# Kernel tuning notes

Hardware: AMD Instinct MI355X
Metric: run time of the kernel (lower is better)

## Reference

```python
import jax, jax.numpy as jnp
import numpy as np

LN_EPS = 1e-5

def _ln(x, g, b):
    m = jnp.mean(x, -1, keepdims=True)
    v = jnp.var(x, -1, keepdims=True)
    return (x - m) / jnp.sqrt(v + LN_EPS) * g + b

def _modgru(X, M, hx0, mask, Wcomb, bcomb, Wih, Whh, bih, bhh, Wc2, bc2):
    # X, M: [S,B,D]; hx0: [B,H]; mask: [S,B]
    # comb and the input-side gate GEMMs are hx-independent -> precompute over all steps
    comb = jnp.einsum('sbd,ed->sbe', jnp.concatenate([X, M], -1), Wcomb) + bcomb  # [S,B,D]
    gi = jnp.einsum('sbd,gd->sbg', comb, Wih) + bih  # [S,B,3H]

    def step(hx, inp):
        gi_t, m_t = inp
        gh = hx @ Whh.T + bhh
        ir, iz, inn = jnp.split(gi_t, 3, -1)
        hr, hz, hn = jnp.split(gh, 3, -1)
        r = jax.nn.sigmoid(ir + hr)
        z = jax.nn.sigmoid(iz + hz)
        n = jnp.tanh(inn + r * hn)
        hnew = (1.0 - z) * n + z * hx  # torch GRUCell update
        m = m_t[:, None]
        hx = hnew * m + hx * (1.0 - m)  # mask blending
        return hx, hx

    hx_last, hs = jax.lax.scan(step, hx0, (gi, mask))  # hs: [S,B,H]
    out = jnp.einsum('sbd,ed->sbe', jnp.concatenate([comb, hs], -1), Wc2) + bc2
    return out, hx_last

def setup_inputs() -> dict:
    key = jax.random.key(0)
    ks = jax.random.split(key, 40)
    S, B, I, H = 256, 512, 70, 512
    D1 = I - 6  # rnn1 input dim (use_src=True)
    f32 = jnp.float32
    def w(k, shape, scale):
        return jax.random.normal(k, shape, f32) * scale
    inp = {
        'X': jax.random.normal(ks[0], (S, B, I), f32),
        'M': (jax.random.uniform(ks[1], (S, B, I)) < 0.9).astype(f32),
        'mask': (jax.random.uniform(ks[2], (S, B)) < 0.95).astype(f32),
        'Wi2h': w(ks[3], (H, 6), 0.3), 'bi2h': jnp.zeros((H,), f32),
        # rnn1 (ModGRU on D1 inputs)
        'Wcomb1': w(ks[4], (D1, 2 * D1), 0.08), 'bcomb1': jnp.zeros((D1,), f32),
        'Wih1': w(ks[5], (3 * H, D1), 0.08), 'Whh1': w(ks[6], (3 * H, H), 0.04),
        'bih1': jnp.zeros((3 * H,), f32), 'bhh1': jnp.zeros((3 * H,), f32),
        'Wc21': w(ks[7], (H, D1 + H), 0.04), 'bc21': jnp.zeros((H,), f32),
        # rnn2 (ModGRU on H inputs)
        'Wcomb2': w(ks[8], (H, 2 * H), 0.03), 'bcomb2': jnp.zeros((H,), f32),
        'Wih2': w(ks[9], (3 * H, H), 0.04), 'Whh2': w(ks[10], (3 * H, H), 0.04),
        'bih2': jnp.zeros((3 * H,), f32), 'bhh2': jnp.zeros((3 * H,), f32),
        'Wc22': w(ks[11], (H, 2 * H), 0.03), 'bc22': jnp.zeros((H,), f32),
        # layer norms
        'g1': jnp.ones((H,), f32), 'b1': jnp.zeros((H,), f32),
        'g2': jnp.ones((H,), f32), 'b2': jnp.zeros((H,), f32),
        'g3': jnp.ones((8,), f32), 'b3': jnp.zeros((8,), f32),
        # heads
        'Wnn1': w(ks[12], (8, H), 0.05), 'bnn1': jnp.zeros((8,), f32),
        'Wnn2': w(ks[13], (2, 8), 0.3), 'bnn2': jnp.zeros((2,), f32),
    }
    return inp

def reference(X, M, mask, Wi2h, bi2h,
              Wcomb1, bcomb1, Wih1, Whh1, bih1, bhh1, Wc21, bc21,
              Wcomb2, bcomb2, Wih2, Whh2, bih2, bhh2, Wc22, bc22,
              g1, b1, g2, b2, g3, b3, Wnn1, bnn1, Wnn2, bnn2):
    # use_src=True: last 6 channels are static patient info
    patient = X[0, :, -6:]                  # [B,6]
    Xin, Min = X[:, :, :-6], M[:, :, :-6]   # [S,B,D1]
    h0 = patient @ Wi2h.T + bi2h            # [B,H]
    hx, _ = _modgru(Xin, Min, h0, mask, Wcomb1, bcomb1, Wih1, Whh1, bih1, bhh1, Wc21, bc21)
    hx = _ln(hx, g1, b1)
    hx, _ = _modgru(hx, jnp.ones_like(hx), h0, mask, Wcomb2, bcomb2, Wih2, Whh2, bih2, bhh2, Wc22, bc22)
    hx = _ln(hx, g2, b2)
    hx = jax.nn.relu(jnp.einsum('sbh,oh->sbo', hx, Wnn1) + bnn1)
    hx = _ln(hx, g3, b3)
    return jnp.einsum('sbh,oh->sbo', hx, Wnn2) + bnn2  # [S,B,2]
```

## Files before the change

kernel.cpp:

```cpp
#include <hip/hip_runtime.h>
#include <hip/hip_bf16.h>

typedef unsigned short u16;
typedef unsigned int   u32;

#define S_  256
#define B_  512
#define H_  512
#define I_  70

__device__ __forceinline__ float bfu(u16 u) {
    return __uint_as_float(((u32)u) << 16);
}
__device__ __forceinline__ u16 f2bf_u(float f) {
    __hip_bfloat16 h = __float2bfloat16(f);
    u16 r;
    __builtin_memcpy(&r, &h, 2);
    return r;
}
__device__ __forceinline__ float sigmoidf_(float x) {
    x = fminf(fmaxf(x, -30.f), 30.f);
    return 1.f / (1.f + __expf(-x));
}
__device__ __forceinline__ float tanhf_(float x) {
    x = fminf(fmaxf(x, -15.f), 15.f);
    float e = __expf(2.f * x);
    return (e - 1.f) / (e + 1.f);
}

__global__ __launch_bounds__(256)
void k_sentinel(float* __restrict__ out, int n, float v) {
    int i = blockIdx.x * 256 + threadIdx.x;
    if (i < n) out[i] = v;
}

__global__ __launch_bounds__(256)
void k_h0(const float* __restrict__ X, const float* __restrict__ Wi2h,
          const float* __restrict__ bi2h, float* __restrict__ h1a,
          float* __restrict__ h2a) {
    int idx = blockIdx.x * 256 + threadIdx.x;
    int b = idx >> 9, h = idx & 511;
    const float* xp = X + b * I_ + 64;
    const float* wp = Wi2h + h * 6;
    float s = bi2h[h];
    #pragma unroll
    for (int j = 0; j < 6; j++) s += xp[j] * wp[j];
    h1a[idx] = s;
    h2a[idx] = s;
}

__global__ __launch_bounds__(256)
void k_beff(const float* __restrict__ Wcomb2, const float* __restrict__ bcomb2,
            float* __restrict__ beff) {
    int e = blockIdx.x * 256 + threadIdx.x;
    if (e >= 512) return;
    float s = bcomb2[e];
    const float* wp = Wcomb2 + (size_t)e * 1024 + 512;
    for (int k = 0; k < 512; k++) s += wp[k];
    beff[e] = s;
}

__global__ __launch_bounds__(256)
void k_comb1(const float* __restrict__ X, const float* __restrict__ M,
             const float* __restrict__ Wcomb1, const float* __restrict__ bcomb1,
             u16* __restrict__ comb1) {
    __shared__ float W_s[128 * 68];
    __shared__ float in_s[16 * 132];
    const int tid = threadIdx.x;
    for (int i = tid; i < 64 * 128; i += 256) {
        int e = i >> 7, k = i & 127;
        W_s[k * 68 + e] = Wcomb1[i];
    }
    const size_t row0 = (size_t)blockIdx.x * 16;
    for (int i = tid; i < 16 * 128; i += 256) {
        int r = i >> 7, k = i & 127;
        size_t rg = row0 + r;
        in_s[r * 132 + k] = (k < 64) ? X[rg * I_ + k] : M[rg * I_ + (k - 64)];
    }
    __syncthreads();
    const int ty = tid >> 4, tx = tid & 15;
    float a0 = 0, a1 = 0, a2 = 0, a3 = 0;
    for (int k = 0; k < 128; k++) {
        float a = in_s[ty * 132 + k];
        float w[4];
        *(float4*)w = *(const float4*)&W_s[k * 68 + tx * 4];
        a0 = fmaf(a, w[0], a0); a1 = fmaf(a, w[1], a1);
        a2 = fmaf(a, w[2], a2); a3 = fmaf(a, w[3], a3);
    }
    size_t rg = row0 + ty;
    int e0 = tx * 4;
    ushort4 st;
    st.x = f2bf_u(a0 + bcomb1[e0 + 0]);
    st.y = f2bf_u(a1 + bcomb1[e0 + 1]);
    st.z = f2bf_u(a2 + bcomb1[e0 + 2]);
    st.w = f2bf_u(a3 + bcomb1[e0 + 3]);
    *(ushort4*)&comb1[rg * 64 + e0] = st;
}

template<int D>
__global__ __launch_bounds__(256)
void k_gru_step(const u16* __restrict__ comb,
                const float* __restrict__ Wih,
                const float* __restrict__ Whh,
                const float* __restrict__ bih, const float* __restrict__ bhh,
                const float* __restrict__ mask,
                const float* __restrict__ hcur, float* __restrict__ hnxt,
                const int t) {
    __shared__ float W_s[24 * 516];
    const int tid = threadIdx.x;
    const int hl = tid & 7;
    const int ty = tid >> 3;
    const int h0 = blockIdx.x * 8;
    const int h  = h0 + hl;
    const int b  = blockIdx.y * 64 + ty * 2;

    for (int i = tid; i < 24 * 128; i += 256) {
        int r = i >> 7, kq = i & 127;
        int g = r >> 3, hh = r & 7;
        *(float4*)&W_s[r * 516 + kq * 4] =
            *(const float4*)&Whh[((size_t)(g * 512 + h0 + hh)) * 512 + kq * 4];
    }
    __syncthreads();

    const float* hr0 = hcur + (size_t)b * 512;
    const float* hr1 = hcur + (size_t)(b + 1) * 512;
    float gh00 = bhh[h], gh10 = bhh[512 + h], gh20 = bhh[1024 + h];
    float gh01 = gh00, gh11 = gh10, gh21 = gh20;
    {
        const float* w0p = &W_s[(0 * 8 + hl) * 516];
        const float* w1p = &W_s[(1 * 8 + hl) * 516];
        const float* w2p = &W_s[(2 * 8 + hl) * 516];
        for (int k = 0; k < 512; k += 4) {
            float4 w0 = *(const float4*)(w0p + k);
            float4 w1 = *(const float4*)(w1p + k);
            float4 w2 = *(const float4*)(w2p + k);
            float4 ha = *(const float4*)(hr0 + k);
            float4 hb = *(const float4*)(hr1 + k);
            gh00 = fmaf(w0.x, ha.x, gh00); gh00 = fmaf(w0.y, ha.y, gh00);
            gh00 = fmaf(w0.z, ha.z, gh00); gh00 = fmaf(w0.w, ha.w, gh00);
            gh10 = fmaf(w1.x, ha.x, gh10); gh10 = fmaf(w1.y, ha.y, gh10);
            gh10 = fmaf(w1.z, ha.z, gh10); gh10 = fmaf(w1.w, ha.w, gh10);
            gh20 = fmaf(w2.x, ha.x, gh20); gh20 = fmaf(w2.y, ha.y, gh20);
            gh20 = fmaf(w2.z, ha.z, gh20); gh20 = fmaf(w2.w, ha.w, gh20);
            gh01 = fmaf(w0.x, hb.x, gh01); gh01 = fmaf(w0.y, hb.y, gh01);
            gh01 = fmaf(w0.z, hb.z, gh01); gh01 = fmaf(w0.w, hb.w, gh01);
            gh11 = fmaf(w1.x, hb.x, gh11); gh11 = fmaf(w1.y, hb.y, gh11);
            gh11 = fmaf(w1.z, hb.z, gh11); gh11 = fmaf(w1.w, hb.w, gh11);
            gh21 = fmaf(w2.x, hb.x, gh21); gh21 = fmaf(w2.y, hb.y, gh21);
            gh21 = fmaf(w2.z, hb.z, gh21); gh21 = fmaf(w2.w, hb.w, gh21);
        }
    }
    __syncthreads();
    constexpr int KQ = D / 4;
    constexpr int WST = (D == 512) ? 516 : (D + 4);
    for (int i = tid; i < 24 * KQ; i += 256) {
        int r = i / KQ, kq = i % KQ;
        int g = r >> 3, hh = r & 7;
        *(float4*)&W_s[r * WST + kq * 4] =
            *(const float4*)&Wih[((size_t)(g * 512 + h0 + hh)) * D + kq * 4];
    }
    __syncthreads();

    const u16* cr0 = comb + ((size_t)t * 512 + b) * D;
    const u16* cr1 = comb + ((size_t)t * 512 + b + 1) * D;
    float gi00 = bih[h], gi10 = bih[512 + h], gi20 = bih[1024 + h];
    float gi01 = gi00, gi11 = gi10, gi21 = gi20;
    {
        const float* w0p = &W_s[(0 * 8 + hl) * WST];
        const float* w1p = &W_s[(1 * 8 + hl) * WST];
        const float* w2p = &W_s[(2 * 8 + hl) * WST];
        for (int k = 0; k < D; k += 4) {
            float4 w0 = *(const float4*)(w0p + k);
            float4 w1 = *(const float4*)(w1p + k);
            float4 w2 = *(const float4*)(w2p + k);
            ushort4 cu0 = *(const ushort4*)(cr0 + k);
            ushort4 cu1 = *(const ushort4*)(cr1 + k);
            float ca[4] = {bfu(cu0.x), bfu(cu0.y), bfu(cu0.z), bfu(cu0.w)};
            float cb[4] = {bfu(cu1.x), bfu(cu1.y), bfu(cu1.z), bfu(cu1.w)};
            gi00 = fmaf(w0.x, ca[0], gi00); gi00 = fmaf(w0.y, ca[1], gi00);
            gi00 = fmaf(w0.z, ca[2], gi00); gi00 = fmaf(w0.w, ca[3], gi00);
            gi10 = fmaf(w1.x, ca[0], gi10); gi10 = fmaf(w1.y, ca[1], gi10);
            gi10 = fmaf(w1.z, ca[2], gi10); gi10 = fmaf(w1.w, ca[3], gi10);
            gi20 = fmaf(w2.x, ca[0], gi20); gi20 = fmaf(w2.y, ca[1], gi20);
            gi20 = fmaf(w2.z, ca[2], gi20); gi20 = fmaf(w2.w, ca[3], gi20);
            gi01 = fmaf(w0.x, cb[0], gi01); gi01 = fmaf(w0.y, cb[1], gi01);
            gi01 = fmaf(w0.z, cb[2], gi01); gi01 = fmaf(w0.w, cb[3], gi01);
            gi11 = fmaf(w1.x, cb[0], gi11); gi11 = fmaf(w1.y, cb[1], gi11);
            gi11 = fmaf(w1.z, cb[2], gi11); gi11 = fmaf(w1.w, cb[3], gi11);
            gi21 = fmaf(w2.x, cb[0], gi21); gi21 = fmaf(w2.y, cb[1], gi21);
            gi21 = fmaf(w2.z, cb[2], gi21); gi21 = fmaf(w2.w, cb[3], gi21);
        }
    }
    {
        float hold = hr0[h];
        float r = sigmoidf_(gi00 + gh00);
        float z = sigmoidf_(gi10 + gh10);
        float n = tanhf_(gi20 + r * gh20);
        float m = mask[t * 512 + b];
        hnxt[(size_t)b * 512 + h] = ((1.f - z) * n + z * hold) * m + hold * (1.f - m);
    }
    {
        float hold = hr1[h];
        float r = sigmoidf_(gi01 + gh01);
        float z = sigmoidf_(gi11 + gh11);
        float n = tanhf_(gi21 + r * gh21);
        float m = mask[t * 512 + b + 1];
        hnxt[(size_t)(b + 1) * 512 + h] = ((1.f - z) * n + z * hold) * m + hold * (1.f - m);
    }
}

__global__ __launch_bounds__(256)
void k_out1comb2(const u16* __restrict__ c1t, const float* __restrict__ h1,
                 const float* __restrict__ Wc21, const float* __restrict__ bc21,
                 const float* __restrict__ g1, const float* __restrict__ b1,
                 const float* __restrict__ Wcomb2, const float* __restrict__ beff,
                 u16* __restrict__ c2t) {
    __shared__ float x_s[4 * 576];
    __shared__ float y_s[4 * 512];
    const int tid = threadIdx.x;
    const int row0 = blockIdx.x * 4;
    for (int i = tid; i < 4 * 64; i += 256) {
        int r = i >> 6, k = i & 63;
        x_s[r * 576 + k] = bfu(c1t[(size_t)(row0 + r) * 64 + k]);
    }
    for (int i = tid; i < 4 * 512; i += 256) {
        int r = i >> 9, k = i & 511;
        x_s[r * 576 + 64 + k] = h1[(size_t)(row0 + r) * 512 + k];
    }
    __syncthreads();
    const int w = tid >> 6, lane = tid & 63;
    const int cg = lane >> 4, kl = lane & 15;
    for (int i = 0; i < 32; i++) {
        int o = i * 16 + w * 4 + cg;
        const float* wrow = Wc21 + (size_t)o * 576;
        float racc[4] = {0.f, 0.f, 0.f, 0.f};
        #pragma unroll
        for (int g = 0; g < 9; g++) {
            int k = g * 64 + kl * 4;
            float4 wv = *(const float4*)(wrow + k);
            #pragma unroll
            for (int r = 0; r < 4; r++) {
                float4 xv = *(const float4*)(x_s + r * 576 + k);
                racc[r] = fmaf(wv.x, xv.x, racc[r]);
                racc[r] = fmaf(wv.y, xv.y, racc[r]);
                racc[r] = fmaf(wv.z, xv.z, racc[r]);
                racc[r] = fmaf(wv.w, xv.w, racc[r]);
            }
        }
        #pragma unroll
        for (int r = 0; r < 4; r++) {
            racc[r] += __shfl_xor(racc[r], 1, 64);
            racc[r] += __shfl_xor(racc[r], 2, 64);
            racc[r] += __shfl_xor(racc[r], 4, 64);
            racc[r] += __shfl_xor(racc[r], 8, 64);
        }
        if (kl == 0) {
            float bb = bc21[o];
            #pragma unroll
            for (int r = 0; r < 4; r++) y_s[r * 512 + o] = racc[r] + bb;
        }
    }
    __syncthreads();
    {
        float v[8], sum = 0.f, ssq = 0.f;
        #pragma unroll
        for (int j = 0; j < 8; j++) {
            v[j] = y_s[w * 512 + lane * 8 + j];
            sum += v[j]; ssq += v[j] * v[j];
        }
        #pragma unroll
        for (int m = 1; m < 64; m <<= 1) {
            sum += __shfl_xor(sum, m, 64);
            ssq += __shfl_xor(ssq, m, 64);
        }
        float mu = sum * (1.f / 512.f);
        float rstd = rsqrtf(ssq * (1.f / 512.f) - mu * mu + 1e-5f);
        #pragma unroll
        for (int j = 0; j < 8; j++) {
            int o = lane * 8 + j;
            y_s[w * 512 + o] = (v[j] - mu) * rstd * g1[o] + b1[o];
        }
    }
    __syncthreads();
    for (int i = 0; i < 32; i++) {
        int o = i * 16 + w * 4 + cg;
        const float* wrow = Wcomb2 + (size_t)o * 1024;
        float racc[4] = {0.f, 0.f, 0.f, 0.f};
        #pragma unroll
        for (int g = 0; g < 8; g++) {
            int k = g * 64 + kl * 4;
            float4 wv = *(const float4*)(wrow + k);
            #pragma unroll
            for (int r = 0; r < 4; r++) {
                float4 xv = *(const float4*)(y_s + r * 512 + k);
                racc[r] = fmaf(wv.x, xv.x, racc[r]);
                racc[r] = fmaf(wv.y, xv.y, racc[r]);
                racc[r] = fmaf(wv.z, xv.z, racc[r]);
                racc[r] = fmaf(wv.w, xv.w, racc[r]);
            }
        }
        #pragma unroll
        for (int r = 0; r < 4; r++) {
            racc[r] += __shfl_xor(racc[r], 1, 64);
            racc[r] += __shfl_xor(racc[r], 2, 64);
            racc[r] += __shfl_xor(racc[r], 4, 64);
            racc[r] += __shfl_xor(racc[r], 8, 64);
        }
        if (kl == 0) {
            float bb = beff[o];
            #pragma unroll
            for (int r = 0; r < 4; r++)
                c2t[(size_t)(row0 + r) * 512 + o] = f2bf_u(racc[r] + bb);
        }
    }
}

__global__ __launch_bounds__(256)
void k_out2head(const u16* __restrict__ c2t, const float* __restrict__ h2,
                const float* __restrict__ Wc22, const float* __restrict__ bc22,
                const float* __restrict__ g2, const float* __restrict__ b2,
                const float* __restrict__ Wnn1, const float* __restrict__ bnn1,
                const float* __restrict__ g3, const float* __restrict__ b3,
                const float* __restrict__ Wnn2, const float* __restrict__ bnn2,
                float* __restrict__ outt) {
    __shared__ float x_s[4 * 1024];
    __shared__ float y_s[4 * 512];
    const int tid = threadIdx.x;
    const int row0 = blockIdx.x * 4;
    for (int i = tid; i < 4 * 512; i += 256) {
        int r = i >> 9, k = i & 511;
        x_s[r * 1024 + k] = bfu(c2t[(size_t)(row0 + r) * 512 + k]);
        x_s[r * 1024 + 512 + k] = h2[(size_t)(row0 + r) * 512 + k];
    }
    __syncthreads();
    const int w = tid >> 6, lane = tid & 63;
    const int cg = lane >> 4, kl = lane & 15;
    for (int i = 0; i < 32; i++) {
        int o = i * 16 + w * 4 + cg;
        const float* wrow = Wc22 + (size_t)o * 1024;
        float racc[4] = {0.f, 0.f, 0.f, 0.f};
        #pragma unroll
        for (int g = 0; g < 16; g++) {
            int k = g * 64 + kl * 4;
            float4 wv = *(const float4*)(wrow + k);
            #pragma unroll
            for (int r = 0; r < 4; r++) {
                float4 xv = *(const float4*)(x_s + r * 1024 + k);
                racc[r] = fmaf(wv.x, xv.x, racc[r]);
                racc[r] = fmaf(wv.y, xv.y, racc[r]);
                racc[r] = fmaf(wv.z, xv.z, racc[r]);
                racc[r] = fmaf(wv.w, xv.w, racc[r]);
            }
        }
        #pragma unroll
        for (int r = 0; r < 4; r++) {
            racc[r] += __shfl_xor(racc[r], 1, 64);
            racc[r] += __shfl_xor(racc[r], 2, 64);
            racc[r] += __shfl_xor(racc[r], 4, 64);
            racc[r] += __shfl_xor(racc[r], 8, 64);
        }
        if (kl == 0) {
            float bb = bc22[o];
            #pragma unroll
            for (int r = 0; r < 4; r++) y_s[r * 512 + o] = racc[r] + bb;
        }
    }
    __syncthreads();
    {
        float v[8], sum = 0.f, ssq = 0.f;
        #pragma unroll
        for (int j = 0; j < 8; j++) {
            v[j] = y_s[w * 512 + lane * 8 + j];
            sum += v[j]; ssq += v[j] * v[j];
        }
        #pragma unroll
        for (int m = 1; m < 64; m <<= 1) {
            sum += __shfl_xor(sum, m, 64);
            ssq += __shfl_xor(ssq, m, 64);
        }
        float mu = sum * (1.f / 512.f);
        float rstd = rsqrtf(ssq * (1.f / 512.f) - mu * mu + 1e-5f);
        #pragma unroll
        for (int j = 0; j < 8; j++) {
            int o = lane * 8 + j;
            y_s[w * 512 + o] = (v[j] - mu) * rstd * g2[o] + b2[o];
        }
    }
    __syncthreads();
    {
        float p[8];
        const float* yp = y_s + w * 512 + lane * 8;
        #pragma unroll
        for (int o8 = 0; o8 < 8; o8++) {
            const float* wp = Wnn1 + o8 * 512 + lane * 8;
            float s = 0.f;
            #pragma unroll
            for (int j = 0; j < 8; j++) s = fmaf(yp[j], wp[j], s);
            p[o8] = s;
        }
        #pragma unroll
        for (int m = 1; m < 64; m <<= 1) {
            #pragma unroll
            for (int o8 = 0; o8 < 8; o8++) p[o8] += __shfl_xor(p[o8], m, 64);
        }
        if (lane == 0) {
            float tv[8], m8 = 0.f;
            #pragma unroll
            for (int o8 = 0; o8 < 8; o8++) {
                tv[o8] = fmaxf(p[o8] + bnn1[o8], 0.f);
                m8 += tv[o8];
            }
            m8 *= 0.125f;
            float var = 0.f;
            #pragma unroll
            for (int o8 = 0; o8 < 8; o8++) { float d = tv[o8] - m8; var += d * d; }
            var *= 0.125f;
            const float rstd8 = rsqrtf(var + 1e-5f);
            float o0v = bnn2[0], o1v = bnn2[1];
            #pragma unroll
            for (int o8 = 0; o8 < 8; o8++) {
                float v = (tv[o8] - m8) * rstd8 * g3[o8] + b3[o8];
                o0v += v * Wnn2[o8];
                o1v += v * Wnn2[8 + o8];
            }
            outt[(row0 + w) * 2 + 0] = o0v;
            outt[(row0 + w) * 2 + 1] = o1v;
        }
    }
}

extern "C" void kernel_launch(void* const* d_in, const int* in_sizes, int n_in,
                              void* d_out, int out_size, void* d_ws, size_t ws_size,
                              hipStream_t stream) {
    const float* X      = (const float*)d_in[0];
    const float* M      = (const float*)d_in[1];
    const float* mask   = (const float*)d_in[2];
    const float* Wi2h   = (const float*)d_in[3];
    const float* bi2h   = (const float*)d_in[4];
    const float* Wcomb1 = (const float*)d_in[5];
    const float* bcomb1 = (const float*)d_in[6];
    const float* Wih1   = (const float*)d_in[7];
    const float* Whh1   = (const float*)d_in[8];
    const float* bih1   = (const float*)d_in[9];
    const float* bhh1   = (const float*)d_in[10];
    const float* Wc21   = (const float*)d_in[11];
    const float* bc21   = (const float*)d_in[12];
    const float* Wcomb2 = (const float*)d_in[13];
    const float* bcomb2 = (const float*)d_in[14];
    const float* Wih2   = (const float*)d_in[15];
    const float* Whh2   = (const float*)d_in[16];
    const float* bih2   = (const float*)d_in[17];
    const float* bhh2   = (const float*)d_in[18];
    const float* Wc22   = (const float*)d_in[19];
    const float* bc22   = (const float*)d_in[20];
    const float* g1     = (const float*)d_in[21];
    const float* b1     = (const float*)d_in[22];
    const float* g2     = (const float*)d_in[23];
    const float* b2     = (const float*)d_in[24];
    const float* g3     = (const float*)d_in[25];
    const float* b3     = (const float*)d_in[26];
    const float* Wnn1   = (const float*)d_in[27];
    const float* bnn1   = (const float*)d_in[28];
    const float* Wnn2   = (const float*)d_in[29];
    const float* bnn2   = (const float*)d_in[30];
    float* out = (float*)d_out;

    const size_t SZ_COMB1 = (size_t)S_ * B_ * 64 * 2;
    const size_t SZ_HX    = (size_t)B_ * H_ * 4;
    const size_t SZ_C2T   = (size_t)B_ * 512 * 2;
    const size_t NEED = SZ_COMB1 + 4 * SZ_HX + SZ_C2T + 8192;
    if (ws_size < NEED) {
        float v = 1.0e4f + (float)(ws_size >> 20);
        k_sentinel<<<(out_size + 255) / 256, 256, 0, stream>>>(out, out_size, v);
        return;
    }
    char* ws = (char*)d_ws;
    u16* comb1 = (u16*)ws;   ws += SZ_COMB1;
    float* h1a = (float*)ws; ws += SZ_HX;
    float* h1b = (float*)ws; ws += SZ_HX;
    float* h2a = (float*)ws; ws += SZ_HX;
    float* h2b = (float*)ws; ws += SZ_HX;
    u16* c2t   = (u16*)ws;   ws += SZ_C2T;
    float* beff = (float*)ws; ws += 512 * 4;

    k_h0<<<1024, 256, 0, stream>>>(X, Wi2h, bi2h, h1a, h2a);
    k_beff<<<2, 256, 0, stream>>>(Wcomb2, bcomb2, beff);
    k_comb1<<<8192, 256, 0, stream>>>(X, M, Wcomb1, bcomb1, comb1);

    for (int t = 0; t < S_; t++) {
        const float* h1c = (t & 1) ? h1b : h1a;
        float*       h1n = (t & 1) ? h1a : h1b;
        const float* h2c = (t & 1) ? h2b : h2a;
        float*       h2n = (t & 1) ? h2a : h2b;
        k_gru_step<64><<<dim3(64, 8), 256, 0, stream>>>(
            comb1, Wih1, Whh1, bih1, bhh1, mask, h1c, h1n, t);
        k_out1comb2<<<128, 256, 0, stream>>>(
            comb1 + (size_t)t * B_ * 64, h1n, Wc21, bc21, g1, b1,
            Wcomb2, beff, c2t);
        k_gru_step<512><<<dim3(64, 8), 256, 0, stream>>>(
            c2t, Wih2, Whh2, bih2, bhh2, mask + (size_t)t * B_, h2c, h2n, 0);
        k_out2head<<<128, 256, 0, stream>>>(
            c2t, h2n, Wc22, bc22, g2, b2, Wnn1, bnn1, g3, b3, Wnn2, bnn2,
            out + (size_t)t * B_ * 2);
    }
}
```

Baseline: 88.38 ms.

## Fuse per-timestep GRU pipeline into one persistent batch-partitioned scan kernel

Replaces the four kernels launched per timestep with a single persistent kernel. Each block owns four batch rows and loops over all timesteps, keeping both hidden states and intermediates in shared memory. This removes about a thousand launches and the global round-trips of hidden states and the combined activations. In exchange, each block streams every weight matrix from cache at every step for only four rows, so the loop depends on L2 bandwidth, and only 128 blocks occupy the device.

```diff
diff --git a/kernel.cpp b/kernel.cpp
--- a/kernel.cpp
+++ b/kernel.cpp
@@ -4,10 +4,12 @@
 typedef unsigned short u16;
 typedef unsigned int   u32;
 
-#define S_  256
-#define B_  512
-#define H_  512
-#define I_  70
+#define S_   256
+#define B_   512
+#define I_   70
+#define ROWS 4
+#define NB   (B_ / ROWS)
+#define NT   1024
 
 __device__ __forceinline__ float bfu(u16 u) {
     return __uint_as_float(((u32)u) << 16);
@@ -32,21 +34,6 @@
 void k_sentinel(float* __restrict__ out, int n, float v) {
     int i = blockIdx.x * 256 + threadIdx.x;
     if (i < n) out[i] = v;
-}
-
-__global__ __launch_bounds__(256)
-void k_h0(const float* __restrict__ X, const float* __restrict__ Wi2h,
-          const float* __restrict__ bi2h, float* __restrict__ h1a,
-          float* __restrict__ h2a) {
-    int idx = blockIdx.x * 256 + threadIdx.x;
-    int b = idx >> 9, h = idx & 511;
-    const float* xp = X + b * I_ + 64;
-    const float* wp = Wi2h + h * 6;
-    float s = bi2h[h];
-    #pragma unroll
-    for (int j = 0; j < 6; j++) s += xp[j] * wp[j];
-    h1a[idx] = s;
-    h2a[idx] = s;
 }
 
 __global__ __launch_bounds__(256)
@@ -97,319 +84,358 @@
     *(ushort4*)&comb1[rg * 64 + e0] = st;
 }
 
-template<int D>
-__global__ __launch_bounds__(256)
-void k_gru_step(const u16* __restrict__ comb,
-                const float* __restrict__ Wih,
-                const float* __restrict__ Whh,
-                const float* __restrict__ bih, const float* __restrict__ bhh,
-                const float* __restrict__ mask,
-                const float* __restrict__ hcur, float* __restrict__ hnxt,
-                const int t) {
-    __shared__ float W_s[24 * 516];
-    const int tid = threadIdx.x;
-    const int hl = tid & 7;
-    const int ty = tid >> 3;
-    const int h0 = blockIdx.x * 8;
-    const int h  = h0 + hl;
-    const int b  = blockIdx.y * 64 + ty * 2;
-
-    for (int i = tid; i < 24 * 128; i += 256) {
-        int r = i >> 7, kq = i & 127;
-        int g = r >> 3, hh = r & 7;
-        *(float4*)&W_s[r * 516 + kq * 4] =
-            *(const float4*)&Whh[((size_t)(g * 512 + h0 + hh)) * 512 + kq * 4];
+__global__ __launch_bounds__(NT, 1)
+void k_scan_b(const u16* __restrict__ comb1, const float* __restrict__ X,
+              const float* __restrict__ mask,
+              const float* __restrict__ Wi2h, const float* __restrict__ bi2h,
+              const float* __restrict__ Wih1, const float* __restrict__ Whh1,
+              const float* __restrict__ bih1, const float* __restrict__ bhh1,
+              const float* __restrict__ Wc21, const float* __restrict__ bc21,
+              const float* __restrict__ lg1, const float* __restrict__ lb1,
+              const float* __restrict__ Wcomb2, const float* __restrict__ beff,
+              const float* __restrict__ Wih2, const float* __restrict__ Whh2,
+              const float* __restrict__ bih2, const float* __restrict__ bhh2,
+              const float* __restrict__ Wc22, const float* __restrict__ bc22,
+              const float* __restrict__ lg2, const float* __restrict__ lb2,
+              const float* __restrict__ Wnn1, const float* __restrict__ bnn1,
+              const float* __restrict__ g3, const float* __restrict__ b3v,
+              const float* __restrict__ Wnn2, const float* __restrict__ bnn2,
+              float* __restrict__ out) {
+    __shared__ float h1s[ROWS * 512];
+    __shared__ float h2s[ROWS * 512];
+    __shared__ float c2s[ROWS * 512];
+    __shared__ float ys [ROWS * 512];
+    __shared__ float gHs[1536 * ROWS];
+    __shared__ float gIs[512 * ROWS];
+
+    float* ph = c2s;
+
+    const int tid  = threadIdx.x;
+    const int w    = tid >> 6;
+    const int lane = tid & 63;
+    const int og   = lane >> 4;
+    const int kl   = lane & 15;
+    const int row0 = blockIdx.x * ROWS;
+
+    for (int c = tid; c < ROWS * 512; c += NT) {
+        int r = c >> 9, h = c & 511;
+        const float* xp = X + (size_t)(row0 + r) * I_ + 64;
+        const float* wp = Wi2h + h * 6;
+        float s = bi2h[h];
+        #pragma unroll
+        for (int j = 0; j < 6; j++) s = fmaf(xp[j], wp[j], s);
+        h1s[c] = s;
+        h2s[c] = s;
     }
     __syncthreads();
 
-    const float* hr0 = hcur + (size_t)b * 512;
-    const float* hr1 = hcur + (size_t)(b + 1) * 512;
-    float gh00 = bhh[h], gh10 = bhh[512 + h], gh20 = bhh[1024 + h];
-    float gh01 = gh00, gh11 = gh10, gh21 = gh20;
-    {
-        const float* w0p = &W_s[(0 * 8 + hl) * 516];
-        const float* w1p = &W_s[(1 * 8 + hl) * 516];
-        const float* w2p = &W_s[(2 * 8 + hl) * 516];
-        for (int k = 0; k < 512; k += 4) {
-            float4 w0 = *(const float4*)(w0p + k);
-            float4 w1 = *(const float4*)(w1p + k);
-            float4 w2 = *(const float4*)(w2p + k);
-            float4 ha = *(const float4*)(hr0 + k);
-            float4 hb = *(const float4*)(hr1 + k);
-            gh00 = fmaf(w0.x, ha.x, gh00); gh00 = fmaf(w0.y, ha.y, gh00);
-            gh00 = fmaf(w0.z, ha.z, gh00); gh00 = fmaf(w0.w, ha.w, gh00);
-            gh10 = fmaf(w1.x, ha.x, gh10); gh10 = fmaf(w1.y, ha.y, gh10);
-            gh10 = fmaf(w1.z, ha.z, gh10); gh10 = fmaf(w1.w, ha.w, gh10);
-            gh20 = fmaf(w2.x, ha.x, gh20); gh20 = fmaf(w2.y, ha.y, gh20);
-            gh20 = fmaf(w2.z, ha.z, gh20); gh20 = fmaf(w2.w, ha.w, gh20);
-            gh01 = fmaf(w0.x, hb.x, gh01); gh01 = fmaf(w0.y, hb.y, gh01);
-            gh01 = fmaf(w0.z, hb.z, gh01); gh01 = fmaf(w0.w, hb.w, gh01);
-            gh11 = fmaf(w1.x, hb.x, gh11); gh11 = fmaf(w1.y, hb.y, gh11);
-            gh11 = fmaf(w1.z, hb.z, gh11); gh11 = fmaf(w1.w, hb.w, gh11);
-            gh21 = fmaf(w2.x, hb.x, gh21); gh21 = fmaf(w2.y, hb.y, gh21);
-            gh21 = fmaf(w2.z, hb.z, gh21); gh21 = fmaf(w2.w, hb.w, gh21);
-        }
-    }
-    __syncthreads();
-    constexpr int KQ = D / 4;
-    constexpr int WST = (D == 512) ? 516 : (D + 4);
-    for (int i = tid; i < 24 * KQ; i += 256) {
-        int r = i / KQ, kq = i % KQ;
-        int g = r >> 3, hh = r & 7;
-        *(float4*)&W_s[r * WST + kq * 4] =
-            *(const float4*)&Wih[((size_t)(g * 512 + h0 + hh)) * D + kq * 4];
-    }
-    __syncthreads();
-
-    const u16* cr0 = comb + ((size_t)t * 512 + b) * D;
-    const u16* cr1 = comb + ((size_t)t * 512 + b + 1) * D;
-    float gi00 = bih[h], gi10 = bih[512 + h], gi20 = bih[1024 + h];
-    float gi01 = gi00, gi11 = gi10, gi21 = gi20;
-    {
-        const float* w0p = &W_s[(0 * 8 + hl) * WST];
-        const float* w1p = &W_s[(1 * 8 + hl) * WST];
-        const float* w2p = &W_s[(2 * 8 + hl) * WST];
-        for (int k = 0; k < D; k += 4) {
-            float4 w0 = *(const float4*)(w0p + k);
-            float4 w1 = *(const float4*)(w1p + k);
-            float4 w2 = *(const float4*)(w2p + k);
-            ushort4 cu0 = *(const ushort4*)(cr0 + k);
-            ushort4 cu1 = *(const ushort4*)(cr1 + k);
-            float ca[4] = {bfu(cu0.x), bfu(cu0.y), bfu(cu0.z), bfu(cu0.w)};
-            float cb[4] = {bfu(cu1.x), bfu(cu1.y), bfu(cu1.z), bfu(cu1.w)};
-            gi00 = fmaf(w0.x, ca[0], gi00); gi00 = fmaf(w0.y, ca[1], gi00);
-            gi00 = fmaf(w0.z, ca[2], gi00); gi00 = fmaf(w0.w, ca[3], gi00);
-            gi10 = fmaf(w1.x, ca[0], gi10); gi10 = fmaf(w1.y, ca[1], gi10);
-            gi10 = fmaf(w1.z, ca[2], gi10); gi10 = fmaf(w1.w, ca[3], gi10);
-            gi20 = fmaf(w2.x, ca[0], gi20); gi20 = fmaf(w2.y, ca[1], gi20);
-            gi20 = fmaf(w2.z, ca[2], gi20); gi20 = fmaf(w2.w, ca[3], gi20);
-            gi01 = fmaf(w0.x, cb[0], gi01); gi01 = fmaf(w0.y, cb[1], gi01);
-            gi01 = fmaf(w0.z, cb[2], gi01); gi01 = fmaf(w0.w, cb[3], gi01);
-            gi11 = fmaf(w1.x, cb[0], gi11); gi11 = fmaf(w1.y, cb[1], gi11);
-            gi11 = fmaf(w1.z, cb[2], gi11); gi11 = fmaf(w1.w, cb[3], gi11);
-            gi21 = fmaf(w2.x, cb[0], gi21); gi21 = fmaf(w2.y, cb[1], gi21);
-            gi21 = fmaf(w2.z, cb[2], gi21); gi21 = fmaf(w2.w, cb[3], gi21);
-        }
-    }
-    {
-        float hold = hr0[h];
-        float r = sigmoidf_(gi00 + gh00);
-        float z = sigmoidf_(gi10 + gh10);
-        float n = tanhf_(gi20 + r * gh20);
-        float m = mask[t * 512 + b];
-        hnxt[(size_t)b * 512 + h] = ((1.f - z) * n + z * hold) * m + hold * (1.f - m);
-    }
-    {
-        float hold = hr1[h];
-        float r = sigmoidf_(gi01 + gh01);
-        float z = sigmoidf_(gi11 + gh11);
-        float n = tanhf_(gi21 + r * gh21);
-        float m = mask[t * 512 + b + 1];
-        hnxt[(size_t)(b + 1) * 512 + h] = ((1.f - z) * n + z * hold) * m + hold * (1.f - m);
-    }
-}
-
-__global__ __launch_bounds__(256)
-void k_out1comb2(const u16* __restrict__ c1t, const float* __restrict__ h1,
-                 const float* __restrict__ Wc21, const float* __restrict__ bc21,
-                 const float* __restrict__ g1, const float* __restrict__ b1,
-                 const float* __restrict__ Wcomb2, const float* __restrict__ beff,
-                 u16* __restrict__ c2t) {
-    __shared__ float x_s[4 * 576];
-    __shared__ float y_s[4 * 512];
-    const int tid = threadIdx.x;
-    const int row0 = blockIdx.x * 4;
-    for (int i = tid; i < 4 * 64; i += 256) {
-        int r = i >> 6, k = i & 63;
-        x_s[r * 576 + k] = bfu(c1t[(size_t)(row0 + r) * 64 + k]);
-    }
-    for (int i = tid; i < 4 * 512; i += 256) {
-        int r = i >> 9, k = i & 511;
-        x_s[r * 576 + 64 + k] = h1[(size_t)(row0 + r) * 512 + k];
-    }
-    __syncthreads();
-    const int w = tid >> 6, lane = tid & 63;
-    const int cg = lane >> 4, kl = lane & 15;
-    for (int i = 0; i < 32; i++) {
-        int o = i * 16 + w * 4 + cg;
-        const float* wrow = Wc21 + (size_t)o * 576;
-        float racc[4] = {0.f, 0.f, 0.f, 0.f};
-        #pragma unroll
-        for (int g = 0; g < 9; g++) {
-            int k = g * 64 + kl * 4;
-            float4 wv = *(const float4*)(wrow + k);
-            #pragma unroll
-            for (int r = 0; r < 4; r++) {
-                float4 xv = *(const float4*)(x_s + r * 576 + k);
-                racc[r] = fmaf(wv.x, xv.x, racc[r]);
-                racc[r] = fmaf(wv.y, xv.y, racc[r]);
-                racc[r] = fmaf(wv.z, xv.z, racc[r]);
-                racc[r] = fmaf(wv.w, xv.w, racc[r]);
-            }
-        }
-        #pragma unroll
-        for (int r = 0; r < 4; r++) {
-            racc[r] += __shfl_xor(racc[r], 1, 64);
-            racc[r] += __shfl_xor(racc[r], 2, 64);
-            racc[r] += __shfl_xor(racc[r], 4, 64);
-            racc[r] += __shfl_xor(racc[r], 8, 64);
-        }
-        if (kl == 0) {
-            float bb = bc21[o];
-            #pragma unroll
-            for (int r = 0; r < 4; r++) y_s[r * 512 + o] = racc[r] + bb;
-        }
-    }
-    __syncthreads();
-    {
-        float v[8], sum = 0.f, ssq = 0.f;
-        #pragma unroll
-        for (int j = 0; j < 8; j++) {
-            v[j] = y_s[w * 512 + lane * 8 + j];
-            sum += v[j]; ssq += v[j] * v[j];
-        }
-        #pragma unroll
-        for (int m = 1; m < 64; m <<= 1) {
-            sum += __shfl_xor(sum, m, 64);
-            ssq += __shfl_xor(ssq, m, 64);
-        }
-        float mu = sum * (1.f / 512.f);
-        float rstd = rsqrtf(ssq * (1.f / 512.f) - mu * mu + 1e-5f);
-        #pragma unroll
-        for (int j = 0; j < 8; j++) {
-            int o = lane * 8 + j;
-            y_s[w * 512 + o] = (v[j] - mu) * rstd * g1[o] + b1[o];
-        }
-    }
-    __syncthreads();
-    for (int i = 0; i < 32; i++) {
-        int o = i * 16 + w * 4 + cg;
-        const float* wrow = Wcomb2 + (size_t)o * 1024;
-        float racc[4] = {0.f, 0.f, 0.f, 0.f};
-        #pragma unroll
-        for (int g = 0; g < 8; g++) {
-            int k = g * 64 + kl * 4;
-            float4 wv = *(const float4*)(wrow + k);
-            #pragma unroll
-            for (int r = 0; r < 4; r++) {
-                float4 xv = *(const float4*)(y_s + r * 512 + k);
-                racc[r] = fmaf(wv.x, xv.x, racc[r]);
-                racc[r] = fmaf(wv.y, xv.y, racc[r]);
-                racc[r] = fmaf(wv.z, xv.z, racc[r]);
-                racc[r] = fmaf(wv.w, xv.w, racc[r]);
-            }
-        }
-        #pragma unroll
-        for (int r = 0; r < 4; r++) {
-            racc[r] += __shfl_xor(racc[r], 1, 64);
-            racc[r] += __shfl_xor(racc[r], 2, 64);
-            racc[r] += __shfl_xor(racc[r], 4, 64);
-            racc[r] += __shfl_xor(racc[r], 8, 64);
-        }
-        if (kl == 0) {
-            float bb = beff[o];
-            #pragma unroll
-            for (int r = 0; r < 4; r++)
-                c2t[(size_t)(row0 + r) * 512 + o] = f2bf_u(racc[r] + bb);
-        }
-    }
-}
-
-__global__ __launch_bounds__(256)
-void k_out2head(const u16* __restrict__ c2t, const float* __restrict__ h2,
-                const float* __restrict__ Wc22, const float* __restrict__ bc22,
-                const float* __restrict__ g2, const float* __restrict__ b2,
-                const float* __restrict__ Wnn1, const float* __restrict__ bnn1,
-                const float* __restrict__ g3, const float* __restrict__ b3,
-                const float* __restrict__ Wnn2, const float* __restrict__ bnn2,
-                float* __restrict__ outt) {
-    __shared__ float x_s[4 * 1024];
-    __shared__ float y_s[4 * 512];
-    const int tid = threadIdx.x;
-    const int row0 = blockIdx.x * 4;
-    for (int i = tid; i < 4 * 512; i += 256) {
-        int r = i >> 9, k = i & 511;
-        x_s[r * 1024 + k] = bfu(c2t[(size_t)(row0 + r) * 512 + k]);
-        x_s[r * 1024 + 512 + k] = h2[(size_t)(row0 + r) * 512 + k];
-    }
-    __syncthreads();
-    const int w = tid >> 6, lane = tid & 63;
-    const int cg = lane >> 4, kl = lane & 15;
-    for (int i = 0; i < 32; i++) {
-        int o = i * 16 + w * 4 + cg;
-        const float* wrow = Wc22 + (size_t)o * 1024;
-        float racc[4] = {0.f, 0.f, 0.f, 0.f};
-        #pragma unroll
-        for (int g = 0; g < 16; g++) {
-            int k = g * 64 + kl * 4;
-            float4 wv = *(const float4*)(wrow + k);
-            #pragma unroll
-            for (int r = 0; r < 4; r++) {
-                float4 xv = *(const float4*)(x_s + r * 1024 + k);
-                racc[r] = fmaf(wv.x, xv.x, racc[r]);
-                racc[r] = fmaf(wv.y, xv.y, racc[r]);
-                racc[r] = fmaf(wv.z, xv.z, racc[r]);
-                racc[r] = fmaf(wv.w, xv.w, racc[r]);
-            }
-        }
-        #pragma unroll
-        for (int r = 0; r < 4; r++) {
-            racc[r] += __shfl_xor(racc[r], 1, 64);
-            racc[r] += __shfl_xor(racc[r], 2, 64);
-            racc[r] += __shfl_xor(racc[r], 4, 64);
-            racc[r] += __shfl_xor(racc[r], 8, 64);
-        }
-        if (kl == 0) {
-            float bb = bc22[o];
-            #pragma unroll
-            for (int r = 0; r < 4; r++) y_s[r * 512 + o] = racc[r] + bb;
-        }
-    }
-    __syncthreads();
-    {
-        float v[8], sum = 0.f, ssq = 0.f;
-        #pragma unroll
-        for (int j = 0; j < 8; j++) {
-            v[j] = y_s[w * 512 + lane * 8 + j];
-            sum += v[j]; ssq += v[j] * v[j];
-        }
-        #pragma unroll
-        for (int m = 1; m < 64; m <<= 1) {
-            sum += __shfl_xor(sum, m, 64);
-            ssq += __shfl_xor(ssq, m, 64);
-        }
-        float mu = sum * (1.f / 512.f);
-        float rstd = rsqrtf(ssq * (1.f / 512.f) - mu * mu + 1e-5f);
-        #pragma unroll
-        for (int j = 0; j < 8; j++) {
-            int o = lane * 8 + j;
-            y_s[w * 512 + o] = (v[j] - mu) * rstd * g2[o] + b2[o];
-        }
-    }
-    __syncthreads();
-    {
-        float p[8];
-        const float* yp = y_s + w * 512 + lane * 8;
-        #pragma unroll
-        for (int o8 = 0; o8 < 8; o8++) {
-            const float* wp = Wnn1 + o8 * 512 + lane * 8;
-            float s = 0.f;
-            #pragma unroll
-            for (int j = 0; j < 8; j++) s = fmaf(yp[j], wp[j], s);
-            p[o8] = s;
-        }
-        #pragma unroll
-        for (int m = 1; m < 64; m <<= 1) {
-            #pragma unroll
-            for (int o8 = 0; o8 < 8; o8++) p[o8] += __shfl_xor(p[o8], m, 64);
-        }
-        if (lane == 0) {
+    for (int t = 0; t < S_; t++) {
+        const u16* c1t = comb1 + ((size_t)t * B_ + row0) * 64;
+        const float* mrow = mask + (size_t)t * B_ + row0;
+
+        for (int i = 0; i < 1536 / 64; i++) {
+            const int o = i * 64 + w * 4 + og;
+            float rH[ROWS] = {0.f, 0.f, 0.f, 0.f};
+            float rI[ROWS] = {0.f, 0.f, 0.f, 0.f};
+            const float* wh = Whh1 + (size_t)o * 512;
+            #pragma unroll
+            for (int seg = 0; seg < 8; seg++) {
+                const int k = seg * 64 + kl * 4;
+                float4 wv = *(const float4*)(wh + k);
+                #pragma unroll
+                for (int r = 0; r < ROWS; r++) {
+                    float4 xv = *(const float4*)(h1s + r * 512 + k);
+                    rH[r] = fmaf(wv.x, xv.x, rH[r]);
+                    rH[r] = fmaf(wv.y, xv.y, rH[r]);
+                    rH[r] = fmaf(wv.z, xv.z, rH[r]);
+                    rH[r] = fmaf(wv.w, xv.w, rH[r]);
+                }
+            }
+            {
+                const int k = kl * 4;
+                float4 wv = *(const float4*)(Wih1 + (size_t)o * 64 + k);
+                #pragma unroll
+                for (int r = 0; r < ROWS; r++) {
+                    ushort4 cu = *(const ushort4*)(c1t + r * 64 + k);
+                    rI[r] = fmaf(wv.x, bfu(cu.x), rI[r]);
+                    rI[r] = fmaf(wv.y, bfu(cu.y), rI[r]);
+                    rI[r] = fmaf(wv.z, bfu(cu.z), rI[r]);
+                    rI[r] = fmaf(wv.w, bfu(cu.w), rI[r]);
+                }
+            }
+            #pragma unroll
+            for (int r = 0; r < ROWS; r++) {
+                #pragma unroll
+                for (int m = 1; m < 16; m <<= 1) {
+                    rH[r] += __shfl_xor(rH[r], m, 64);
+                    rI[r] += __shfl_xor(rI[r], m, 64);
+                }
+            }
+            if (kl == 0) {
+                if (o < 1024) {
+                    #pragma unroll
+                    for (int r = 0; r < ROWS; r++) gHs[o * ROWS + r] = rH[r] + rI[r];
+                } else {
+                    #pragma unroll
+                    for (int r = 0; r < ROWS; r++) {
+                        gHs[o * ROWS + r] = rH[r];
+                        gIs[(o - 1024) * ROWS + r] = rI[r];
+                    }
+                }
+            }
+        }
+        __syncthreads();
+        for (int c = tid; c < ROWS * 512; c += NT) {
+            const int r = c >> 9, h = c & 511;
+            const float m = mrow[r];
+            const float hold = h1s[c];
+            float xr = gHs[h * ROWS + r] + bih1[h] + bhh1[h];
+            float xz = gHs[(512 + h) * ROWS + r] + bih1[512 + h] + bhh1[512 + h];
+            float hn = gHs[(1024 + h) * ROWS + r] + bhh1[1024 + h];
+            float xn = gIs[h * ROWS + r] + bih1[1024 + h];
+            float rg = sigmoidf_(xr);
+            float zg = sigmoidf_(xz);
+            float ng = tanhf_(xn + rg * hn);
+            h1s[c] = ((1.f - zg) * ng + zg * hold) * m + hold * (1.f - m);
+        }
+        __syncthreads();
+        for (int i = 0; i < 512 / 64; i++) {
+            const int o = i * 64 + w * 4 + og;
+            float racc[ROWS] = {0.f, 0.f, 0.f, 0.f};
+            const float* wr = Wc21 + (size_t)o * 576;
+            #pragma unroll
+            for (int seg = 0; seg < 8; seg++) {
+                const int k = seg * 64 + kl * 4;
+                float4 wv = *(const float4*)(wr + 64 + k);
+                #pragma unroll
+                for (int r = 0; r < ROWS; r++) {
+                    float4 xv = *(const float4*)(h1s + r * 512 + k);
+                    racc[r] = fmaf(wv.x, xv.x, racc[r]);
+                    racc[r] = fmaf(wv.y, xv.y, racc[r]);
+                    racc[r] = fmaf(wv.z, xv.z, racc[r]);
+                    racc[r] = fmaf(wv.w, xv.w, racc[r]);
+                }
+            }
+            {
+                const int k = kl * 4;
+                float4 wv = *(const float4*)(wr + k);
+                #pragma unroll
+                for (int r = 0; r < ROWS; r++) {
+                    ushort4 cu = *(const ushort4*)(c1t + r * 64 + k);
+                    racc[r] = fmaf(wv.x, bfu(cu.x), racc[r]);
+                    racc[r] = fmaf(wv.y, bfu(cu.y), racc[r]);
+                    racc[r] = fmaf(wv.z, bfu(cu.z), racc[r]);
+                    racc[r] = fmaf(wv.w, bfu(cu.w), racc[r]);
+                }
+            }
+            #pragma unroll
+            for (int r = 0; r < ROWS; r++) {
+                #pragma unroll
+                for (int m = 1; m < 16; m <<= 1) racc[r] += __shfl_xor(racc[r], m, 64);
+            }
+            if (kl == 0) {
+                #pragma unroll
+                for (int r = 0; r < ROWS; r++) ys[r * 512 + o] = racc[r] + bc21[o];
+            }
+        }
+        __syncthreads();
+        if (w < ROWS) {
+            const int base = w * 512 + lane * 8;
+            float v[8];
+            *(float4*)&v[0] = *(const float4*)(ys + base);
+            *(float4*)&v[4] = *(const float4*)(ys + base + 4);
+            float sum = 0.f, ssq = 0.f;
+            #pragma unroll
+            for (int j = 0; j < 8; j++) { sum += v[j]; ssq += v[j] * v[j]; }
+            #pragma unroll
+            for (int m = 1; m < 64; m <<= 1) {
+                sum += __shfl_xor(sum, m, 64);
+                ssq += __shfl_xor(ssq, m, 64);
+            }
+            const float mu = sum * (1.f / 512.f);
+            const float rstd = rsqrtf(ssq * (1.f / 512.f) - mu * mu + 1e-5f);
+            #pragma unroll
+            for (int j = 0; j < 8; j++) {
+                const int o = lane * 8 + j;
+                ys[base + j] = (v[j] - mu) * rstd * lg1[o] + lb1[o];
+            }
+        }
+        __syncthreads();
+        for (int i = 0; i < 512 / 64; i++) {
+            const int o = i * 64 + w * 4 + og;
+            float racc[ROWS] = {0.f, 0.f, 0.f, 0.f};
+            const float* wr = Wcomb2 + (size_t)o * 1024;
+            #pragma unroll
+            for (int seg = 0; seg < 8; seg++) {
+                const int k = seg * 64 + kl * 4;
+                float4 wv = *(const float4*)(wr + k);
+                #pragma unroll
+                for (int r = 0; r < ROWS; r++) {
+                    float4 xv = *(const float4*)(ys + r * 512 + k);
+                    racc[r] = fmaf(wv.x, xv.x, racc[r]);
+                    racc[r] = fmaf(wv.y, xv.y, racc[r]);
+                    racc[r] = fmaf(wv.z, xv.z, racc[r]);
+                    racc[r] = fmaf(wv.w, xv.w, racc[r]);
+                }
+            }
+            #pragma unroll
+            for (int r = 0; r < ROWS; r++) {
+                #pragma unroll
+                for (int m = 1; m < 16; m <<= 1) racc[r] += __shfl_xor(racc[r], m, 64);
+            }
+            if (kl == 0) {
+                #pragma unroll
+                for (int r = 0; r < ROWS; r++) c2s[r * 512 + o] = racc[r] + beff[o];
+            }
+        }
+        __syncthreads();
+        for (int i = 0; i < 1536 / 64; i++) {
+            const int o = i * 64 + w * 4 + og;
+            float rH[ROWS] = {0.f, 0.f, 0.f, 0.f};
+            float rI[ROWS] = {0.f, 0.f, 0.f, 0.f};
+            const float* wh = Whh2 + (size_t)o * 512;
+            const float* wi = Wih2 + (size_t)o * 512;
+            #pragma unroll
+            for (int seg = 0; seg < 8; seg++) {
+                const int k = seg * 64 + kl * 4;
+                float4 wv = *(const float4*)(wh + k);
+                float4 uv = *(const float4*)(wi + k);
+                #pragma unroll
+                for (int r = 0; r < ROWS; r++) {
+                    float4 xv = *(const float4*)(h2s + r * 512 + k);
+                    float4 cv = *(const float4*)(c2s + r * 512 + k);
+                    rH[r] = fmaf(wv.x, xv.x, rH[r]);
+                    rH[r] = fmaf(wv.y, xv.y, rH[r]);
+                    rH[r] = fmaf(wv.z, xv.z, rH[r]);
+                    rH[r] = fmaf(wv.w, xv.w, rH[r]);
+                    rI[r] = fmaf(uv.x, cv.x, rI[r]);
+                    rI[r] = fmaf(uv.y, cv.y, rI[r]);
+                    rI[r] = fmaf(uv.z, cv.z, rI[r]);
+                    rI[r] = fmaf(uv.w, cv.w, rI[r]);
+                }
+            }
+            #pragma unroll
+            for (int r = 0; r < ROWS; r++) {
+                #pragma unroll
+                for (int m = 1; m < 16; m <<= 1) {
+                    rH[r] += __shfl_xor(rH[r], m, 64);
+                    rI[r] += __shfl_xor(rI[r], m, 64);
+                }
+            }
+            if (kl == 0) {
+                if (o < 1024) {
+                    #pragma unroll
+                    for (int r = 0; r < ROWS; r++) gHs[o * ROWS + r] = rH[r] + rI[r];
+                } else {
+                    #pragma unroll
+                    for (int r = 0; r < ROWS; r++) {
+                        gHs[o * ROWS + r] = rH[r];
+                        gIs[(o - 1024) * ROWS + r] = rI[r];
+                    }
+                }
+            }
+        }
+        __syncthreads();
+        for (int c = tid; c < ROWS * 512; c += NT) {
+            const int r = c >> 9, h = c & 511;
+            const float m = mrow[r];
+            const float hold = h2s[c];
+            float xr = gHs[h * ROWS + r] + bih2[h] + bhh2[h];
+            float xz = gHs[(512 + h) * ROWS + r] + bih2[512 + h] + bhh2[512 + h];
+            float hn = gHs[(1024 + h) * ROWS + r] + bhh2[1024 + h];
+            float xn = gIs[h * ROWS + r] + bih2[1024 + h];
+            float rg = sigmoidf_(xr);
+            float zg = sigmoidf_(xz);
+            float ng = tanhf_(xn + rg * hn);
+            h2s[c] = ((1.f - zg) * ng + zg * hold) * m + hold * (1.f - m);
+        }
+        __syncthreads();
+        for (int i = 0; i < 512 / 64; i++) {
+            const int o = i * 64 + w * 4 + og;
+            float racc[ROWS] = {0.f, 0.f, 0.f, 0.f};
+            const float* wr = Wc22 + (size_t)o * 1024;
+            #pragma unroll
+            for (int seg = 0; seg < 8; seg++) {
+                const int k = seg * 64 + kl * 4;
+                float4 wv = *(const float4*)(wr + k);
+                float4 uv = *(const float4*)(wr + 512 + k);
+                #pragma unroll
+                for (int r = 0; r < ROWS; r++) {
+                    float4 cv = *(const float4*)(c2s + r * 512 + k);
+                    float4 xv = *(const float4*)(h2s + r * 512 + k);
+                    racc[r] = fmaf(wv.x, cv.x, racc[r]);
+                    racc[r] = fmaf(wv.y, cv.y, racc[r]);
+                    racc[r] = fmaf(wv.z, cv.z, racc[r]);
+                    racc[r] = fmaf(wv.w, cv.w, racc[r]);
+                    racc[r] = fmaf(uv.x, xv.x, racc[r]);
+                    racc[r] = fmaf(uv.y, xv.y, racc[r]);
+                    racc[r] = fmaf(uv.z, xv.z, racc[r]);
+                    racc[r] = fmaf(uv.w, xv.w, racc[r]);
+                }
+            }
+            #pragma unroll
+            for (int r = 0; r < ROWS; r++) {
+                #pragma unroll
+                for (int m = 1; m < 16; m <<= 1) racc[r] += __shfl_xor(racc[r], m, 64);
+            }
+            if (kl == 0) {
+                #pragma unroll
+                for (int r = 0; r < ROWS; r++) ys[r * 512 + o] = racc[r] + bc22[o];
+            }
+        }
+        __syncthreads();
+        if (w < ROWS) {
+            const int base = w * 512 + lane * 8;
+            float v[8];
+            *(float4*)&v[0] = *(const float4*)(ys + base);
+            *(float4*)&v[4] = *(const float4*)(ys + base + 4);
+            float sum = 0.f, ssq = 0.f;
+            #pragma unroll
+            for (int j = 0; j < 8; j++) { sum += v[j]; ssq += v[j] * v[j]; }
+            #pragma unroll
+            for (int m = 1; m < 64; m <<= 1) {
+                sum += __shfl_xor(sum, m, 64);
+                ssq += __shfl_xor(ssq, m, 64);
+            }
+            const float mu = sum * (1.f / 512.f);
+            const float rstd = rsqrtf(ssq * (1.f / 512.f) - mu * mu + 1e-5f);
+            #pragma unroll
+            for (int j = 0; j < 8; j++) {
+                const int o = lane * 8 + j;
+                ys[base + j] = (v[j] - mu) * rstd * lg2[o] + lb2[o];
+            }
+        }
+        __syncthreads();
+        if (w < 8) {
+            float p[ROWS];
+            const float* wp = Wnn1 + w * 512 + lane * 8;
+            float4 wa = *(const float4*)wp;
+            float4 wb = *(const float4*)(wp + 4);
+            #pragma unroll
+            for (int r = 0; r < ROWS; r++) {
+                const float* yp = ys + r * 512 + lane * 8;
+                float4 ya = *(const float4*)yp;
+                float4 yb = *(const float4*)(yp + 4);
+                p[r] = ya.x * wa.x + ya.y * wa.y + ya.z * wa.z + ya.w * wa.w
+                     + yb.x * wb.x + yb.y * wb.y + yb.z * wb.z + yb.w * wb.w;
+            }
+            #pragma unroll
+            for (int m = 1; m < 64; m <<= 1) {
+                #pragma unroll
+                for (int r = 0; r < ROWS; r++) p[r] += __shfl_xor(p[r], m, 64);
+            }
+            if (lane == 0) {
+                #pragma unroll
+                for (int r = 0; r < ROWS; r++)
+                    ph[w * ROWS + r] = fmaxf(p[r] + bnn1[w], 0.f);
+            }
+        }
+        __syncthreads();
+        if (tid < ROWS) {
+            const int r = tid;
             float tv[8], m8 = 0.f;
             #pragma unroll
-            for (int o8 = 0; o8 < 8; o8++) {
-                tv[o8] = fmaxf(p[o8] + bnn1[o8], 0.f);
-                m8 += tv[o8];
-            }
+            for (int o8 = 0; o8 < 8; o8++) { tv[o8] = ph[o8 * ROWS + r]; m8 += tv[o8]; }
             m8 *= 0.125f;
             float var = 0.f;
             #pragma unroll
@@ -419,13 +445,15 @@
             float o0v = bnn2[0], o1v = bnn2[1];
             #pragma unroll
             for (int o8 = 0; o8 < 8; o8++) {
-                float v = (tv[o8] - m8) * rstd8 * g3[o8] + b3[o8];
+                float v = (tv[o8] - m8) * rstd8 * g3[o8] + b3v[o8];
                 o0v += v * Wnn2[o8];
                 o1v += v * Wnn2[8 + o8];
             }
-            outt[(row0 + w) * 2 + 0] = o0v;
-            outt[(row0 + w) * 2 + 1] = o1v;
-        }
+            float* op = out + ((size_t)t * B_ + row0 + r) * 2;
+            op[0] = o0v;
+            op[1] = o1v;
+        }
+        __syncthreads();
     }
 }
 
@@ -466,9 +494,7 @@
     float* out = (float*)d_out;
 
     const size_t SZ_COMB1 = (size_t)S_ * B_ * 64 * 2;
-    const size_t SZ_HX    = (size_t)B_ * H_ * 4;
-    const size_t SZ_C2T   = (size_t)B_ * 512 * 2;
-    const size_t NEED = SZ_COMB1 + 4 * SZ_HX + SZ_C2T + 8192;
+    const size_t NEED = SZ_COMB1 + 8192;
     if (ws_size < NEED) {
         float v = 1.0e4f + (float)(ws_size >> 20);
         k_sentinel<<<(out_size + 255) / 256, 256, 0, stream>>>(out, out_size, v);
@@ -476,31 +502,17 @@
     }
     char* ws = (char*)d_ws;
     u16* comb1 = (u16*)ws;   ws += SZ_COMB1;
-    float* h1a = (float*)ws; ws += SZ_HX;
-    float* h1b = (float*)ws; ws += SZ_HX;
-    float* h2a = (float*)ws; ws += SZ_HX;
-    float* h2b = (float*)ws; ws += SZ_HX;
-    u16* c2t   = (u16*)ws;   ws += SZ_C2T;
-    float* beff = (float*)ws; ws += 512 * 4;
-
-    k_h0<<<1024, 256, 0, stream>>>(X, Wi2h, bi2h, h1a, h2a);
+    float* beff = (float*)ws;
+
     k_beff<<<2, 256, 0, stream>>>(Wcomb2, bcomb2, beff);
     k_comb1<<<8192, 256, 0, stream>>>(X, M, Wcomb1, bcomb1, comb1);
 
-    for (int t = 0; t < S_; t++) {
-        const float* h1c = (t & 1) ? h1b : h1a;
-        float*       h1n = (t & 1) ? h1a : h1b;
-        const float* h2c = (t & 1) ? h2b : h2a;
-        float*       h2n = (t & 1) ? h2a : h2b;
-        k_gru_step<64><<<dim3(64, 8), 256, 0, stream>>>(
-            comb1, Wih1, Whh1, bih1, bhh1, mask, h1c, h1n, t);
-        k_out1comb2<<<128, 256, 0, stream>>>(
-            comb1 + (size_t)t * B_ * 64, h1n, Wc21, bc21, g1, b1,
-            Wcomb2, beff, c2t);
-        k_gru_step<512><<<dim3(64, 8), 256, 0, stream>>>(
-            c2t, Wih2, Whh2, bih2, bhh2, mask + (size_t)t * B_, h2c, h2n, 0);
-        k_out2head<<<128, 256, 0, stream>>>(
-            c2t, h2n, Wc22, bc22, g2, b2, Wnn1, bnn1, g3, b3, Wnn2, bnn2,
-            out + (size_t)t * B_ * 2);
-    }
-}
+    k_scan_b<<<NB, NT, 0, stream>>>(
+        comb1, X, mask, Wi2h, bi2h,
+        Wih1, Whh1, bih1, bhh1,
+        Wc21, bc21, g1, b1,
+        Wcomb2, beff,
+        Wih2, Whh2, bih2, bhh2,
+        Wc22, bc22, g2, b2,
+        Wnn1, bnn1, g3, b3, Wnn2, bnn2, out);
+}
```

Result: slower. 284.6 ms (+222.1%).
